# Kernel optimization log

Hardware: AMD Instinct MI355X
Metric: run time of the kernel (lower is better)

## Reference

```python
import jax, jax.numpy as jnp
import numpy as np

N = 50000   # nodes
E = 800000  # edges
D = 256     # input feature dim
H = 128     # hidden size
OUT = 40    # output classes


def setup_inputs() -> dict:
    key = jax.random.key(0)
    ks = jax.random.split(key, 10)
    s = 0.05
    return {
        "x": jax.random.normal(ks[0], (N, D), jnp.float32),
        "edge_index": jax.random.randint(ks[1], (2, E), 0, N, dtype=jnp.int64),
        "W0": jax.random.normal(ks[2], (D, H), jnp.float32) * s,
        "b0": jnp.zeros((H,), jnp.float32),
        "W1": jax.random.normal(ks[3], (H, H), jnp.float32) * s,
        "b1": jnp.zeros((H,), jnp.float32),
        "W2": jax.random.normal(ks[4], (H, H), jnp.float32) * s,
        "b2": jnp.zeros((H,), jnp.float32),
        "Wout": jax.random.normal(ks[5], (H * 3, OUT), jnp.float32) * s,
        "bout": jnp.zeros((OUT,), jnp.float32),
    }


def _gcn_norm(edge_index, n):
    # PyG gcn_norm: add self-loops, symmetric D^-1/2 (A+I) D^-1/2 weights
    row, col = edge_index[0], edge_index[1]
    loop = jnp.arange(n, dtype=edge_index.dtype)
    row = jnp.concatenate([row, loop])
    col = jnp.concatenate([col, loop])
    deg = jax.ops.segment_sum(jnp.ones_like(col, jnp.float32), col, num_segments=n)
    dinv = jnp.where(deg > 0, jax.lax.rsqrt(jnp.maximum(deg, 1.0)), 0.0)
    norm = dinv[row] * dinv[col]  # [E+N]
    return row, col, norm


def _gcn_conv(x, W, b, row, col, norm, n):
    h = x @ W                                   # dense transform first (PyG order)
    msg = h[row] * norm[:, None]                # gather source feats, scale
    out = jax.ops.segment_sum(msg, col, num_segments=n)  # scatter-aggregate
    return out + b


def reference(x, edge_index, W0, b0, W1, b1, W2, b2, Wout, bout):
    n = x.shape[0]
    row, col, norm = _gcn_norm(edge_index, n)
    x1 = jax.nn.relu(_gcn_conv(x, W0, b0, row, col, norm, n))
    x2 = jax.nn.relu(_gcn_conv(x1, W1, b1, row, col, norm, n))
    x3 = jax.nn.relu(_gcn_conv(x2, W2, b2, row, col, norm, n))
    xs = jnp.concatenate([x1, x2, x3], axis=-1)  # JumpingKnowledge 'cat'
    return xs @ Wout + bout
```

## Files before the change

### kernel.cpp

```cpp
#include <hip/hip_runtime.h>

#define HID 128
#define NOUT 40
#define SCAN_B 256
#define NWIN 8

typedef __attribute__((ext_vector_type(8))) short bf16x8;
typedef __attribute__((ext_vector_type(4))) float f32x4;

__device__ inline float bf2f(unsigned int u) {
    unsigned int t = u << 16;
    float f;
    __builtin_memcpy(&f, &t, 4);
    return f;
}
__device__ inline unsigned short f2bf(float f) {
    unsigned int x;
    __builtin_memcpy(&x, &f, 4);
    unsigned int r = (x + 0x7fffu + ((x >> 16) & 1u)) >> 16;
    return (unsigned short)r;
}
__device__ inline bf16x8 pack_bf8(float4 u, float4 v) {
    bf16x8 r;
    r[0] = (short)f2bf(u.x); r[1] = (short)f2bf(u.y);
    r[2] = (short)f2bf(u.z); r[3] = (short)f2bf(u.w);
    r[4] = (short)f2bf(v.x); r[5] = (short)f2bf(v.y);
    r[6] = (short)f2bf(v.z); r[7] = (short)f2bf(v.w);
    return r;
}

__global__ void prep_kernel(const unsigned int* __restrict__ e, int* __restrict__ flag,
                            int* __restrict__ deg, int N) {
    if (blockIdx.x == 0 && threadIdx.x < 64) {
        unsigned int v = e[2 * threadIdx.x + 1];
        unsigned long long ball = __ballot(v == 0u);
        if (threadIdx.x == 0) *flag = (ball == ~0ull) ? 1 : 0;
    }
    int stride = gridDim.x * blockDim.x;
    for (int j = blockIdx.x * blockDim.x + threadIdx.x; j < N; j += stride) deg[j] = 0;
}

__global__ void degwt_kernel(const void* __restrict__ eix, const int* __restrict__ flag,
                             int* __restrict__ deg, int E, int gE,
                             const float* __restrict__ W0, const float* __restrict__ W1,
                             const float* __restrict__ W2, const float* __restrict__ Wo,
                             unsigned short* __restrict__ W0t, unsigned short* __restrict__ W1t,
                             unsigned short* __restrict__ W2t, unsigned short* __restrict__ Wot) {
    if (blockIdx.x < gE) {
        int i = blockIdx.x * blockDim.x + threadIdx.x;
        if (i >= E) return;
        int f = *flag;
        int c = f ? (int)(((const long long*)eix)[(size_t)E + i]) : ((const int*)eix)[(size_t)E + i];
        atomicAdd(&deg[c], 1);
    } else {
        int idx = (blockIdx.x - gE) * blockDim.x + threadIdx.x;
        const int s0 = 128 * 256, s1 = 128 * 128, s2 = 128 * 128, s3 = 48 * 384;
        if (idx < s0) {
            int n = idx >> 8, k = idx & 255;
            W0t[idx] = f2bf(W0[(size_t)k * 128 + n]);
        } else if ((idx -= s0) < s1) {
            int n = idx >> 7, k = idx & 127;
            W1t[idx] = f2bf(W1[(size_t)k * 128 + n]);
        } else if ((idx -= s1) < s2) {
            int n = idx >> 7, k = idx & 127;
            W2t[idx] = f2bf(W2[(size_t)k * 128 + n]);
        } else if ((idx -= s2) < s3) {
            int n = idx / 384, k = idx - n * 384;
            Wot[idx] = (n < NOUT) ? f2bf(Wo[(size_t)k * NOUT + n]) : (unsigned short)0;
        }
    }
}

__global__ void scan1_kernel(const int* __restrict__ deg, int* __restrict__ offs,
                             int* __restrict__ bsum, float* __restrict__ dinv, int N) {
    __shared__ int s[SCAN_B];
    int i = blockIdx.x * SCAN_B + threadIdx.x;
    int v = (i < N) ? deg[i] : 0;
    if (i < N) dinv[i] = rsqrtf((float)v + 1.0f);
    s[threadIdx.x] = v;
    __syncthreads();
    for (int d = 1; d < SCAN_B; d <<= 1) {
        int t = (threadIdx.x >= d) ? s[threadIdx.x - d] : 0;
        __syncthreads();
        s[threadIdx.x] += t;
        __syncthreads();
    }
    if (i < N) offs[i] = s[threadIdx.x] - v;
    if (threadIdx.x == SCAN_B - 1) bsum[blockIdx.x] = s[SCAN_B - 1];
}

__global__ void scan2_kernel(int* __restrict__ bsum, int nb) {
    __shared__ int s[SCAN_B];
    int v = (threadIdx.x < nb) ? bsum[threadIdx.x] : 0;
    s[threadIdx.x] = v;
    __syncthreads();
    for (int d = 1; d < SCAN_B; d <<= 1) {
        int t = (threadIdx.x >= d) ? s[threadIdx.x - d] : 0;
        __syncthreads();
        s[threadIdx.x] += t;
        __syncthreads();
    }
    if (threadIdx.x < nb) bsum[threadIdx.x] = s[threadIdx.x] - v;
}

__global__ void scan3_kernel(int* __restrict__ offs, const int* __restrict__ bsum,
                             int* __restrict__ cursor, int N, int E) {
    int i = blockIdx.x * SCAN_B + threadIdx.x;
    if (i < N) {
        int v = offs[i] + bsum[blockIdx.x];
        offs[i] = v;
        cursor[i] = v;
    }
    if (blockIdx.x == 0 && threadIdx.x == 0) offs[N] = E;
}

__global__ __launch_bounds__(256) void fill_csr_kernel(
    const void* __restrict__ eix, const int* __restrict__ flag,
    const float* __restrict__ dinv, int* __restrict__ cursor,
    int2* __restrict__ pkd, int E, int N) {
    const int wn = blockIdx.x & (NWIN - 1);
    const int slice = blockIdx.x >> 3;
    const int nslice = gridDim.x >> 3;
    const int wsz = (N + NWIN - 1) / NWIN;
    const int lo = wn * wsz, hi = lo + wsz;
    const int f = *flag;
    const int stride = nslice * 256;
    for (int i = slice * 256 + threadIdx.x; i < E; i += stride) {
        int r, c;
        if (f) {
            r = (int)(((const long long*)eix)[i]);
            c = (int)(((const long long*)eix)[(size_t)E + i]);
        } else {
            r = ((const int*)eix)[i];
            c = ((const int*)eix)[(size_t)E + i];
        }
        if (c >= lo && c < hi) {
            int p = atomicAdd(&cursor[c], 1);
            int2 rec;
            rec.x = r;
            rec.y = __float_as_int(dinv[r] * dinv[c]);
            pkd[p] = rec;
        }
    }
}

template <bool AF32, int K>
__global__ __launch_bounds__(256) void gemm_mfma_kernel(
    const void* __restrict__ Ap, const unsigned short* __restrict__ Wt,
    unsigned short* __restrict__ H, int M) {
    __shared__ unsigned short Bs[128 * 128];
    const int tid = threadIdx.x;
    const int lane = tid & 63;
    const int w = tid >> 6;
    const int lr = lane & 15;
    const int ko = lane >> 4;
    const int bm = blockIdx.x * 128;

    f32x4 acc[2][8];
#pragma unroll
    for (int i = 0; i < 2; ++i)
#pragma unroll
        for (int j = 0; j < 8; ++j) acc[i][j] = (f32x4){0.f, 0.f, 0.f, 0.f};

    size_t aoff[2];
#pragma unroll
    for (int mi = 0; mi < 2; ++mi) {
        int R = bm + w * 32 + mi * 16 + lr;
        if (R >= M) R = M - 1;
        aoff[mi] = (size_t)R * K + ko * 8;
    }

#pragma unroll
    for (int kp = 0; kp < K; kp += 128) {
        for (int c = tid; c < 128 * 16; c += 256) {
            int row = c >> 4;
            int ch = c & 15;
            int sch = ch ^ (row & 7);
            *(bf16x8*)(Bs + row * 128 + sch * 8) =
                *(const bf16x8*)(Wt + (size_t)row * K + kp + ch * 8);
        }
        __syncthreads();

#pragma unroll
        for (int k0 = 0; k0 < 128; k0 += 32) {
            bf16x8 a[2], b[8];
#pragma unroll
            for (int mi = 0; mi < 2; ++mi) {
                if constexpr (AF32) {
                    const float* p = (const float*)Ap + aoff[mi] + kp + k0;
                    float4 u = *(const float4*)p;
                    float4 v = *(const float4*)(p + 4);
                    a[mi] = pack_bf8(u, v);
                } else {
                    a[mi] = *(const bf16x8*)((const unsigned short*)Ap + aoff[mi] + kp + k0);
                }
            }
            const int chb = (k0 >> 3) + ko;
#pragma unroll
            for (int ni = 0; ni < 8; ++ni) {
                int row = ni * 16 + lr;
                b[ni] = *(const bf16x8*)(Bs + row * 128 + ((chb ^ (row & 7)) * 8));
            }
#pragma unroll
            for (int mi = 0; mi < 2; ++mi)
#pragma unroll
                for (int ni = 0; ni < 8; ++ni)
                    acc[mi][ni] = __builtin_amdgcn_mfma_f32_16x16x32_bf16(a[mi], b[ni], acc[mi][ni], 0, 0, 0);
        }
        __syncthreads();
    }

    unsigned short* Cw = Bs + w * (16 * 136);
#pragma unroll
    for (int mi = 0; mi < 2; ++mi) {
#pragma unroll
        for (int ni = 0; ni < 8; ++ni)
#pragma unroll
            for (int r = 0; r < 4; ++r)
                Cw[(ko * 4 + r) * 136 + ni * 16 + lr] = f2bf(acc[mi][ni][r]);
        const int R0 = bm + w * 32 + mi * 16;
#pragma unroll
        for (int p = 0; p < 4; ++p) {
            int row = p * 4 + (lane >> 4);
            int col = (lane & 15) * 8;
            int Ro = R0 + row;
            if (Ro < M) {
                uint4 v = *(const uint4*)(Cw + row * 136 + col);
                *(uint4*)(H + (size_t)Ro * HID + col) = v;
            }
        }
    }
}

__global__ __launch_bounds__(256) void agg_csr_kernel(
    const unsigned int* __restrict__ h32, const int* __restrict__ offs,
    const int2* __restrict__ pkd, const float* __restrict__ dinv,
    const float* __restrict__ bias, unsigned int* __restrict__ xo, int N) {
    const int lane = threadIdx.x & 63;
    const int n = (blockIdx.x * blockDim.x + threadIdx.x) >> 6;
    if (n >= N) return;
    const float d = dinv[n];
    unsigned int sv = h32[(size_t)n * 64 + lane];
    float ax = bf2f(sv & 0xffff) * (d * d) + bias[2 * lane + 0];
    float ay = bf2f(sv >> 16) * (d * d) + bias[2 * lane + 1];
    int e = offs[n];
    const int e1 = offs[n + 1];

    for (; e + 16 <= e1; e += 16) {
        int2 pk[16];
        unsigned int v[16];
#pragma unroll
        for (int j = 0; j < 16; ++j) pk[j] = pkd[e + j];
#pragma unroll
        for (int j = 0; j < 16; ++j) v[j] = h32[(size_t)pk[j].x * 64 + lane];
#pragma unroll
        for (int j = 0; j < 16; ++j) {
            float wv = __int_as_float(pk[j].y);
            ax += bf2f(v[j] & 0xffff) * wv;
            ay += bf2f(v[j] >> 16) * wv;
        }
    }
    for (; e + 4 <= e1; e += 4) {
        int2 pk[4];
        unsigned int v[4];
#pragma unroll
        for (int j = 0; j < 4; ++j) pk[j] = pkd[e + j];
#pragma unroll
        for (int j = 0; j < 4; ++j) v[j] = h32[(size_t)pk[j].x * 64 + lane];
#pragma unroll
        for (int j = 0; j < 4; ++j) {
            float wv = __int_as_float(pk[j].y);
            ax += bf2f(v[j] & 0xffff) * wv;
            ay += bf2f(v[j] >> 16) * wv;
        }
    }
    for (; e < e1; ++e) {
        int2 pk = pkd[e];
        unsigned int v = h32[(size_t)pk.x * 64 + lane];
        float wv = __int_as_float(pk.y);
        ax += bf2f(v & 0xffff) * wv;
        ay += bf2f(v >> 16) * wv;
    }
    ax = fmaxf(ax, 0.f);
    ay = fmaxf(ay, 0.f);
    xo[(size_t)n * 64 + lane] = (unsigned int)f2bf(ax) | ((unsigned int)f2bf(ay) << 16);
}

__global__ __launch_bounds__(256) void head_mfma_kernel(
    const unsigned short* __restrict__ x1, const unsigned short* __restrict__ x2,
    const unsigned short* __restrict__ x3, const unsigned short* __restrict__ Wt,
    const float* __restrict__ bout, float* __restrict__ out, int M) {
    const int tid = threadIdx.x;
    const int lane = tid & 63;
    const int w = tid >> 6;
    const int lr = lane & 15;
    const int ko = lane >> 4;
    const int bm = blockIdx.x * 64;
    int R = bm + w * 16 + lr;
    if (R >= M) R = M - 1;
    const unsigned short* xs[3] = {x1, x2, x3};

    f32x4 acc[3];
#pragma unroll
    for (int i = 0; i < 3; ++i) acc[i] = (f32x4){0.f, 0.f, 0.f, 0.f};

#pragma unroll
    for (int s = 0; s < 3; ++s) {
        const unsigned short* xp = xs[s] + (size_t)R * HID + ko * 8;
#pragma unroll
        for (int c = 0; c < 4; ++c) {
            bf16x8 a = *(const bf16x8*)(xp + c * 32);
#pragma unroll
            for (int ni = 0; ni < 3; ++ni) {
                bf16x8 b = *(const bf16x8*)(Wt + (size_t)(ni * 16 + lr) * 384 + s * 128 + c * 32 + ko * 8);
                acc[ni] = __builtin_amdgcn_mfma_f32_16x16x32_bf16(a, b, acc[ni], 0, 0, 0);
            }
        }
    }

    int Rb = bm + w * 16 + ko * 4;
#pragma unroll
    for (int r = 0; r < 4; ++r) {
        int Ro = Rb + r;
        if (Ro < M) {
#pragma unroll
            for (int ni = 0; ni < 3; ++ni) {
                int C = ni * 16 + lr;
                if (C < NOUT) out[(size_t)Ro * NOUT + C] = acc[ni][r] + bout[C];
            }
        }
    }
}

static inline size_t align_up(size_t x, size_t a) { return (x + a - 1) / a * a; }

extern "C" void kernel_launch(void* const* d_in, const int* in_sizes, int n_in,
                              void* d_out, int out_size, void* d_ws, size_t ws_size,
                              hipStream_t stream) {
    const float* x    = (const float*)d_in[0];
    const void*  eix  = d_in[1];
    const float* W0   = (const float*)d_in[2];
    const float* b0   = (const float*)d_in[3];
    const float* W1   = (const float*)d_in[4];
    const float* b1   = (const float*)d_in[5];
    const float* W2   = (const float*)d_in[6];
    const float* b2   = (const float*)d_in[7];
    const float* Wout = (const float*)d_in[8];
    const float* bout = (const float*)d_in[9];
    float* out = (float*)d_out;

    const int D = 256;
    const int N = in_sizes[0] / D;
    const int E = in_sizes[1] / 2;

    char* w = (char*)d_ws;
    size_t off = 0;
    int* deg = (int*)(w + off);             off = align_up(off + (size_t)N * 4, 256);
    float* dinv = (float*)(w + off);        off = align_up(off + (size_t)N * 4, 256);
    int* offs = (int*)(w + off);            off = align_up(off + (size_t)(N + 1) * 4, 256);
    int* cursor = (int*)(w + off);          off = align_up(off + (size_t)N * 4, 256);
    int* bsum = (int*)(w + off);            off = align_up(off + 1024 * 4, 256);
    int* flag = (int*)(w + off);            off = align_up(off + 16, 256);
    int2* pkd = (int2*)(w + off);           off = align_up(off + (size_t)E * 8, 256);
    unsigned short* h   = (unsigned short*)(w + off); off = align_up(off + (size_t)N * HID * 2, 256);
    unsigned short* x1b = (unsigned short*)(w + off); off = align_up(off + (size_t)N * HID * 2, 256);
    unsigned short* x2b = (unsigned short*)(w + off); off = align_up(off + (size_t)N * HID * 2, 256);
    unsigned short* x3b = (unsigned short*)(w + off); off = align_up(off + (size_t)N * HID * 2, 256);
    unsigned short* W0t = (unsigned short*)(w + off); off = align_up(off + (size_t)HID * 256 * 2, 256);
    unsigned short* W1t = (unsigned short*)(w + off); off = align_up(off + (size_t)HID * HID * 2, 256);
    unsigned short* W2t = (unsigned short*)(w + off); off = align_up(off + (size_t)HID * HID * 2, 256);
    unsigned short* Wot = (unsigned short*)(w + off); off = align_up(off + (size_t)48 * 384 * 2, 256);
    (void)ws_size;

    prep_kernel<<<128, 256, 0, stream>>>((const unsigned int*)eix, flag, deg, N);

    const int gE = (E + 255) / 256;
    const int wtTot = 128 * 256 + 128 * 128 + 128 * 128 + 48 * 384;
    const int gW = (wtTot + 255) / 256;
    degwt_kernel<<<gE + gW, 256, 0, stream>>>(eix, flag, deg, E, gE,
                                              W0, W1, W2, Wout, W0t, W1t, W2t, Wot);

    const int nb = (N + SCAN_B - 1) / SCAN_B;
    scan1_kernel<<<nb, SCAN_B, 0, stream>>>(deg, offs, bsum, dinv, N);
    scan2_kernel<<<1, SCAN_B, 0, stream>>>(bsum, nb);
    scan3_kernel<<<nb, SCAN_B, 0, stream>>>(offs, bsum, cursor, N, E);
    fill_csr_kernel<<<NWIN * 256, 256, 0, stream>>>(eix, flag, dinv, cursor, pkd, E, N);

    const int gGemm = (N + 127) / 128;
    const int gAgg = (N * 64 + 255) / 256;

    gemm_mfma_kernel<true, 256><<<gGemm, 256, 0, stream>>>(x, W0t, h, N);
    agg_csr_kernel<<<gAgg, 256, 0, stream>>>((const unsigned int*)h, offs, pkd, dinv, b0, (unsigned int*)x1b, N);
    gemm_mfma_kernel<false, 128><<<gGemm, 256, 0, stream>>>(x1b, W1t, h, N);
    agg_csr_kernel<<<gAgg, 256, 0, stream>>>((const unsigned int*)h, offs, pkd, dinv, b1, (unsigned int*)x2b, N);
    gemm_mfma_kernel<false, 128><<<gGemm, 256, 0, stream>>>(x2b, W2t, h, N);
    agg_csr_kernel<<<gAgg, 256, 0, stream>>>((const unsigned int*)h, offs, pkd, dinv, b2, (unsigned int*)x3b, N);
    head_mfma_kernel<<<(N + 63) / 64, 256, 0, stream>>>(x1b, x2b, x3b, Wot, bout, out, N);
}
```

Measured before the change: 359.7 us.

## Store CSR source indices only, compute edge weights on the fly, merge scan passes

The CSR build now writes only the source index per edge (4 bytes instead of an 8-byte index+weight pair). Aggregation recomputes each edge weight as dinv[src]*dinv[dst] with an extra gather from the small dinv array. The second and third scan kernels are merged so every block redundantly rescans the block sums and applies its own base, which saves one launch. The GEMM epilogue's LDS row pitch also changes from 136 to 144 to alter the bank-conflict pattern. The trade-off is an extra random dinv load per edge against halved CSR traffic in each of the three aggregation passes.

```diff
diff --git a/kernel.cpp b/kernel.cpp
--- a/kernel.cpp
+++ b/kernel.cpp
@@ -89,7 +89,8 @@
     if (threadIdx.x == SCAN_B - 1) bsum[blockIdx.x] = s[SCAN_B - 1];
 }
 
-__global__ void scan2_kernel(int* __restrict__ bsum, int nb) {
+__global__ void scan23_kernel(int* __restrict__ offs, const int* __restrict__ bsum,
+                              int* __restrict__ cursor, int N, int E, int nb) {
     __shared__ int s[SCAN_B];
     int v = (threadIdx.x < nb) ? bsum[threadIdx.x] : 0;
     s[threadIdx.x] = v;
@@ -100,24 +101,19 @@
         s[threadIdx.x] += t;
         __syncthreads();
     }
-    if (threadIdx.x < nb) bsum[threadIdx.x] = s[threadIdx.x] - v;
-}
-
-__global__ void scan3_kernel(int* __restrict__ offs, const int* __restrict__ bsum,
-                             int* __restrict__ cursor, int N, int E) {
+    const int base = (blockIdx.x == 0) ? 0 : s[blockIdx.x - 1];
     int i = blockIdx.x * SCAN_B + threadIdx.x;
     if (i < N) {
-        int v = offs[i] + bsum[blockIdx.x];
-        offs[i] = v;
-        cursor[i] = v;
+        int o = offs[i] + base;
+        offs[i] = o;
+        cursor[i] = o;
     }
     if (blockIdx.x == 0 && threadIdx.x == 0) offs[N] = E;
 }
 
 __global__ __launch_bounds__(256) void fill_csr_kernel(
     const void* __restrict__ eix, const int* __restrict__ flag,
-    const float* __restrict__ dinv, int* __restrict__ cursor,
-    int2* __restrict__ pkd, int E, int N) {
+    int* __restrict__ cursor, int* __restrict__ csrc, int E, int N) {
     const int wn = blockIdx.x & (NWIN - 1);
     const int slice = blockIdx.x >> 3;
     const int nslice = gridDim.x >> 3;
@@ -136,10 +132,7 @@
         }
         if (c >= lo && c < hi) {
             int p = atomicAdd(&cursor[c], 1);
-            int2 rec;
-            rec.x = r;
-            rec.y = __float_as_int(dinv[r] * dinv[c]);
-            pkd[p] = rec;
+            csrc[p] = r;
         }
     }
 }
@@ -210,14 +203,14 @@
         __syncthreads();
     }
 
-    unsigned short* Cw = Bs + w * (16 * 136);
+    unsigned short* Cw = Bs + w * (16 * 144);
 #pragma unroll
     for (int mi = 0; mi < 2; ++mi) {
 #pragma unroll
         for (int ni = 0; ni < 8; ++ni)
 #pragma unroll
             for (int r = 0; r < 4; ++r)
-                Cw[(ko * 4 + r) * 136 + ni * 16 + lr] = f2bf(acc[mi][ni][r]);
+                Cw[(ko * 4 + r) * 144 + ni * 16 + lr] = f2bf(acc[mi][ni][r]);
         const int R0 = bm + w * 32 + mi * 16;
 #pragma unroll
         for (int p = 0; p < 4; ++p) {
@@ -225,7 +218,7 @@
             int col = (lane & 15) * 8;
             int Ro = R0 + row;
             if (Ro < M) {
-                uint4 v = *(const uint4*)(Cw + row * 136 + col);
+                uint4 v = *(const uint4*)(Cw + row * 144 + col);
                 *(uint4*)(H + (size_t)Ro * HID + col) = v;
             }
         }
@@ -234,7 +227,7 @@
 
 __global__ __launch_bounds__(256) void agg_csr_kernel(
     const unsigned int* __restrict__ h32, const int* __restrict__ offs,
-    const int2* __restrict__ pkd, const float* __restrict__ dinv,
+    const int* __restrict__ csrc, const float* __restrict__ dinv,
     const float* __restrict__ bias, unsigned int* __restrict__ xo, int N) {
     const int lane = threadIdx.x & 63;
     const int n = (blockIdx.x * blockDim.x + threadIdx.x) >> 6;
@@ -247,39 +240,45 @@
     const int e1 = offs[n + 1];
 
     for (; e + 16 <= e1; e += 16) {
-        int2 pk[16];
+        int r[16];
         unsigned int v[16];
-#pragma unroll
-        for (int j = 0; j < 16; ++j) pk[j] = pkd[e + j];
-#pragma unroll
-        for (int j = 0; j < 16; ++j) v[j] = h32[(size_t)pk[j].x * 64 + lane];
+        float wv[16];
+#pragma unroll
+        for (int j = 0; j < 16; ++j) r[j] = csrc[e + j];
+#pragma unroll
+        for (int j = 0; j < 16; ++j) v[j] = h32[(size_t)r[j] * 64 + lane];
+#pragma unroll
+        for (int j = 0; j < 16; ++j) wv[j] = dinv[r[j]];
 #pragma unroll
         for (int j = 0; j < 16; ++j) {
-            float wv = __int_as_float(pk[j].y);
-            ax += bf2f(v[j] & 0xffff) * wv;
-            ay += bf2f(v[j] >> 16) * wv;
+            float wd = wv[j] * d;
+            ax += bf2f(v[j] & 0xffff) * wd;
+            ay += bf2f(v[j] >> 16) * wd;
         }
     }
     for (; e + 4 <= e1; e += 4) {
-        int2 pk[4];
+        int r[4];
         unsigned int v[4];
-#pragma unroll
-        for (int j = 0; j < 4; ++j) pk[j] = pkd[e + j];
-#pragma unroll
-        for (int j = 0; j < 4; ++j) v[j] = h32[(size_t)pk[j].x * 64 + lane];
+        float wv[4];
+#pragma unroll
+        for (int j = 0; j < 4; ++j) r[j] = csrc[e + j];
+#pragma unroll
+        for (int j = 0; j < 4; ++j) v[j] = h32[(size_t)r[j] * 64 + lane];
+#pragma unroll
+        for (int j = 0; j < 4; ++j) wv[j] = dinv[r[j]];
 #pragma unroll
         for (int j = 0; j < 4; ++j) {
-            float wv = __int_as_float(pk[j].y);
-            ax += bf2f(v[j] & 0xffff) * wv;
-            ay += bf2f(v[j] >> 16) * wv;
+            float wd = wv[j] * d;
+            ax += bf2f(v[j] & 0xffff) * wd;
+            ay += bf2f(v[j] >> 16) * wd;
         }
     }
     for (; e < e1; ++e) {
-        int2 pk = pkd[e];
-        unsigned int v = h32[(size_t)pk.x * 64 + lane];
-        float wv = __int_as_float(pk.y);
-        ax += bf2f(v & 0xffff) * wv;
-        ay += bf2f(v >> 16) * wv;
+        int r = csrc[e];
+        unsigned int v = h32[(size_t)r * 64 + lane];
+        float wd = dinv[r] * d;
+        ax += bf2f(v & 0xffff) * wd;
+        ay += bf2f(v >> 16) * wd;
     }
     ax = fmaxf(ax, 0.f);
     ay = fmaxf(ay, 0.f);
@@ -361,7 +360,7 @@
     int* cursor = (int*)(w + off);          off = align_up(off + (size_t)N * 4, 256);
     int* bsum = (int*)(w + off);            off = align_up(off + 1024 * 4, 256);
     int* flag = (int*)(w + off);            off = align_up(off + 16, 256);
-    int2* pkd = (int2*)(w + off);           off = align_up(off + (size_t)E * 8, 256);
+    int* csrc = (int*)(w + off);            off = align_up(off + (size_t)E * 4, 256);
     unsigned short* h   = (unsigned short*)(w + off); off = align_up(off + (size_t)N * HID * 2, 256);
     unsigned short* x1b = (unsigned short*)(w + off); off = align_up(off + (size_t)N * HID * 2, 256);
     unsigned short* x2b = (unsigned short*)(w + off); off = align_up(off + (size_t)N * HID * 2, 256);
@@ -382,18 +381,17 @@
 
     const int nb = (N + SCAN_B - 1) / SCAN_B;
     scan1_kernel<<<nb, SCAN_B, 0, stream>>>(deg, offs, bsum, dinv, N);
-    scan2_kernel<<<1, SCAN_B, 0, stream>>>(bsum, nb);
-    scan3_kernel<<<nb, SCAN_B, 0, stream>>>(offs, bsum, cursor, N, E);
-    fill_csr_kernel<<<NWIN * 256, 256, 0, stream>>>(eix, flag, dinv, cursor, pkd, E, N);
+    scan23_kernel<<<nb, SCAN_B, 0, stream>>>(offs, bsum, cursor, N, E, nb);
+    fill_csr_kernel<<<NWIN * 256, 256, 0, stream>>>(eix, flag, cursor, csrc, E, N);
 
     const int gGemm = (N + 127) / 128;
     const int gAgg = (N * 64 + 255) / 256;
 
     gemm_mfma_kernel<true, 256><<<gGemm, 256, 0, stream>>>(x, W0t, h, N);
-    agg_csr_kernel<<<gAgg, 256, 0, stream>>>((const unsigned int*)h, offs, pkd, dinv, b0, (unsigned int*)x1b, N);
+    agg_csr_kernel<<<gAgg, 256, 0, stream>>>((const unsigned int*)h, offs, csrc, dinv, b0, (unsigned int*)x1b, N);
     gemm_mfma_kernel<false, 128><<<gGemm, 256, 0, stream>>>(x1b, W1t, h, N);
-    agg_csr_kernel<<<gAgg, 256, 0, stream>>>((const unsigned int*)h, offs, pkd, dinv, b1, (unsigned int*)x2b, N);
+    agg_csr_kernel<<<gAgg, 256, 0, stream>>>((const unsigned int*)h, offs, csrc, dinv, b1, (unsigned int*)x2b, N);
     gemm_mfma_kernel<false, 128><<<gGemm, 256, 0, stream>>>(x2b, W2t, h, N);
-    agg_csr_kernel<<<gAgg, 256, 0, stream>>>((const unsigned int*)h, offs, pkd, dinv, b2, (unsigned int*)x3b, N);
+    agg_csr_kernel<<<gAgg, 256, 0, stream>>>((const unsigned int*)h, offs, csrc, dinv, b2, (unsigned int*)x3b, N);
     head_mfma_kernel<<<(N + 63) / 64, 256, 0, stream>>>(x1b, x2b, x3b, Wot, bout, out, N);
 }
```

After: 351.9 us. 1.02x faster.
